# Kernel optimization log

Hardware: AMD Instinct MI355X
Metric: run time of the kernel (lower is better)

## Reference

```python
import jax, jax.numpy as jnp
import numpy as np

# Production-scale perfect decision-tree ensemble (Hummingbird perf_tree_trav layout)
B, F, T, D, C = 16384, 256, 512, 7, 4  # batch, features, trees, internal levels below root, classes


def setup_inputs() -> dict:
    key = jax.random.key(0)
    k = jax.random.split(key, 6)
    total = T * (2 ** (D + 1) - 2)  # concatenated per-level node/bias tables, level l has T*2^l entries
    return {
        "x": jax.random.normal(k[0], (B, F), dtype=jnp.float32),
        "root_nodes": jax.random.randint(k[1], (T,), 0, F, dtype=jnp.int32),
        "root_biases": jax.random.normal(k[2], (T,), dtype=jnp.float32),
        "tree_indices": jnp.arange(T, dtype=jnp.int32) * 2,
        "nodes_flat": jax.random.randint(k[3], (total,), 0, F, dtype=jnp.int32),
        "biases_flat": jax.random.normal(k[4], (total,), dtype=jnp.float32),
        "leaf_nodes": jax.random.normal(k[5], (T * 2 ** (D + 1), C), dtype=jnp.float32),
    }


def reference(x, root_nodes, root_biases, tree_indices, nodes_flat, biases_flat, leaf_nodes):
    # Root level: compare each tree's root feature against its bias. decision_cond = less (lt).
    # tree_indices = t*2 offsets indices into the flat level-1 table of size 2T;
    # the offset doubles along with the level size via `2*idx + cond`.
    idx = (x[:, root_nodes] < root_biases).astype(jnp.int32) + tree_indices  # [B, T]
    off = 0
    for l in range(1, D + 1):  # static loop over tree depth
        size = T << l
        lvl_nodes = nodes_flat[off:off + size]
        lvl_biases = biases_flat[off:off + size]
        feat_idx = lvl_nodes[idx]                          # [B, T] feature ids for current nodes
        feats = jnp.take_along_axis(x, feat_idx, axis=1)   # [B, T] per-sample feature gather
        idx = 2 * idx + (feats < lvl_biases[idx]).astype(jnp.int32)
        off += size
    leaves = leaf_nodes[idx]                               # [B, T, C]
    return leaves.sum(axis=1)                              # [B, C]
```

## Files before the change

kernel.cpp:

```cpp
#include <hip/hip_runtime.h>

#define BB 16384
#define FF 256
#define TT 512
#define DD 7

#define XS 257

constexpr int S_   = 32;
constexpr int NT_  = 512;
constexpr int NTG  = NT_ / S_;
constexpr int TPT  = TT / NTG;
constexpr int NP   = 8;
constexpr int NJ   = TPT / NP;
constexpr int NPACK = TT * ((1 << (DD + 1)) - 2);

__global__ void pack_nodes_kernel(const int* __restrict__ nf,
                                  const float* __restrict__ bf,
                                  int2* __restrict__ tp, int n) {
    int i = blockIdx.x * 256 + threadIdx.x;
    if (i < n) tp[i] = make_int2(nf[i], __float_as_int(bf[i]));
}

template<bool PACKED>
__global__ __launch_bounds__(NT_, 4)
void tree_traverse_kernel(const float* __restrict__ x,
                          const int*   __restrict__ root_nodes,
                          const float* __restrict__ root_biases,
                          const int*   __restrict__ nodes_flat,
                          const float* __restrict__ biases_flat,
                          const float* __restrict__ leaf_nodes,
                          const int2*  __restrict__ tp,
                          float*       __restrict__ out)
{
    __shared__ float x_s[S_ * XS];

    const int tid = threadIdx.x;
    const int s   = tid & (S_ - 1);
    const int tg  = tid / S_;
    const int s0  = blockIdx.x * S_;

    {
        const float4* xg = (const float4*)(x + (size_t)s0 * FF);
        const int r = tid >> 4;
        const int v = tid & 15;
        #pragma unroll
        for (int c = 0; c < 4; ++c) {
            const float4 q = xg[r * (FF / 4) + v + 16 * c];
            const int base = r * XS + (v + 16 * c) * 4;
            x_s[base + 0] = q.x; x_s[base + 1] = q.y;
            x_s[base + 2] = q.z; x_s[base + 3] = q.w;
        }
    }
    __syncthreads();

    const int xb = s * XS;
    const float4* leaf4 = (const float4*)leaf_nodes;
    float a0 = 0.f, a1 = 0.f, a2 = 0.f, a3 = 0.f;

    #pragma unroll 1
    for (int j = 0; j < NJ; ++j) {
        const int tbase = tg * TPT + j * NP;

        int p[NP];
        #pragma unroll
        for (int k = 0; k < NP; ++k) {
            const int t  = tbase + k;
            const int rn = root_nodes[t];
            const float rb = root_biases[t];
            p[k] = (x_s[xb + rn] < rb) ? 1 : 0;
        }

        #pragma unroll
        for (int l = 1; l <= DD; ++l) {
            const int lbase = TT * ((1 << l) - 2);
            #pragma unroll
            for (int k = 0; k < NP; ++k) {
                const int t = tbase + k;
                const int e = lbase + (t << l) + p[k];
                int   fi; float bi;
                if (PACKED) {
                    const int2 nb = tp[e];
                    fi = nb.x; bi = __int_as_float(nb.y);
                } else {
                    fi = nodes_flat[e]; bi = biases_flat[e];
                }
                const float ft = x_s[xb + fi];
                p[k] = 2 * p[k] + ((ft < bi) ? 1 : 0);
            }
        }

        #pragma unroll
        for (int k = 0; k < NP; ++k) {
            const int t = tbase + k;
            const float4 lf = leaf4[(t << (DD + 1)) + p[k]];
            a0 += lf.x; a1 += lf.y; a2 += lf.z; a3 += lf.w;
        }
    }

    __syncthreads();
    float* red = x_s;
    red[tid * 4 + 0] = a0; red[tid * 4 + 1] = a1;
    red[tid * 4 + 2] = a2; red[tid * 4 + 3] = a3;
    __syncthreads();
    if (tid < S_) {
        float o0 = 0.f, o1 = 0.f, o2 = 0.f, o3 = 0.f;
        #pragma unroll
        for (int g = 0; g < NTG; ++g) {
            const int jj = (g * S_ + tid) * 4;
            o0 += red[jj + 0]; o1 += red[jj + 1];
            o2 += red[jj + 2]; o3 += red[jj + 3];
        }
        ((float4*)out)[s0 + tid] = make_float4(o0, o1, o2, o3);
    }
}

extern "C" void kernel_launch(void* const* d_in, const int* in_sizes, int n_in,
                              void* d_out, int out_size, void* d_ws, size_t ws_size,
                              hipStream_t stream) {
    const float* x           = (const float*)d_in[0];
    const int*   root_nodes  = (const int*)  d_in[1];
    const float* root_biases = (const float*)d_in[2];
    const int*   nodes_flat  = (const int*)  d_in[4];
    const float* biases_flat = (const float*)d_in[5];
    const float* leaf_nodes  = (const float*)d_in[6];
    float*       out         = (float*)d_out;

    const bool packed = ws_size >= (size_t)NPACK * sizeof(int2);
    int2* tp = (int2*)d_ws;

    if (packed) {
        pack_nodes_kernel<<<(NPACK + 255) / 256, 256, 0, stream>>>(
            nodes_flat, biases_flat, tp, NPACK);
        tree_traverse_kernel<true><<<BB / S_, NT_, 0, stream>>>(
            x, root_nodes, root_biases, nodes_flat, biases_flat, leaf_nodes, tp, out);
    } else {
        tree_traverse_kernel<false><<<BB / S_, NT_, 0, stream>>>(
            x, root_nodes, root_biases, nodes_flat, biases_flat, leaf_nodes, tp, out);
    }
}
```

Baseline: 117.6 us.

## Split trees across two grid halves with atomic output reduction, drop node packing

Splits the tree ensemble into two halves along a second grid dimension, so each block traverses 256 trees for its 32 samples. Partial sums are combined with atomicAdd into an output that is zeroed by a memset first. The separate pack kernel that interleaved node ids and biases is removed in favour of two separate loads, and launch bounds are raised to 8 blocks per CU. This doubles the number of blocks, which helps occupancy and load balance, but loads the x tile into shared memory twice and adds atomics plus a memset.

```diff
diff --git a/kernel.cpp b/kernel.cpp
--- a/kernel.cpp
+++ b/kernel.cpp
@@ -10,27 +10,18 @@
 constexpr int S_   = 32;
 constexpr int NT_  = 512;
 constexpr int NTG  = NT_ / S_;
-constexpr int TPT  = TT / NTG;
+constexpr int HT   = TT / 2;
+constexpr int TPT  = HT / NTG;
 constexpr int NP   = 8;
 constexpr int NJ   = TPT / NP;
-constexpr int NPACK = TT * ((1 << (DD + 1)) - 2);
 
-__global__ void pack_nodes_kernel(const int* __restrict__ nf,
-                                  const float* __restrict__ bf,
-                                  int2* __restrict__ tp, int n) {
-    int i = blockIdx.x * 256 + threadIdx.x;
-    if (i < n) tp[i] = make_int2(nf[i], __float_as_int(bf[i]));
-}
-
-template<bool PACKED>
-__global__ __launch_bounds__(NT_, 4)
+__global__ __launch_bounds__(NT_, 8)
 void tree_traverse_kernel(const float* __restrict__ x,
                           const int*   __restrict__ root_nodes,
                           const float* __restrict__ root_biases,
                           const int*   __restrict__ nodes_flat,
                           const float* __restrict__ biases_flat,
                           const float* __restrict__ leaf_nodes,
-                          const int2*  __restrict__ tp,
                           float*       __restrict__ out)
 {
     __shared__ float x_s[S_ * XS];
@@ -39,6 +30,7 @@
     const int s   = tid & (S_ - 1);
     const int tg  = tid / S_;
     const int s0  = blockIdx.x * S_;
+    const int h0  = blockIdx.y * HT;
 
     {
         const float4* xg = (const float4*)(x + (size_t)s0 * FF);
@@ -60,7 +52,7 @@
 
     #pragma unroll 1
     for (int j = 0; j < NJ; ++j) {
-        const int tbase = tg * TPT + j * NP;
+        const int tbase = h0 + tg * TPT + j * NP;
 
         int p[NP];
         #pragma unroll
@@ -78,13 +70,8 @@
             for (int k = 0; k < NP; ++k) {
                 const int t = tbase + k;
                 const int e = lbase + (t << l) + p[k];
-                int   fi; float bi;
-                if (PACKED) {
-                    const int2 nb = tp[e];
-                    fi = nb.x; bi = __int_as_float(nb.y);
-                } else {
-                    fi = nodes_flat[e]; bi = biases_flat[e];
-                }
+                const int   fi = nodes_flat[e];
+                const float bi = biases_flat[e];
                 const float ft = x_s[xb + fi];
                 p[k] = 2 * p[k] + ((ft < bi) ? 1 : 0);
             }
@@ -103,15 +90,14 @@
     red[tid * 4 + 0] = a0; red[tid * 4 + 1] = a1;
     red[tid * 4 + 2] = a2; red[tid * 4 + 3] = a3;
     __syncthreads();
-    if (tid < S_) {
-        float o0 = 0.f, o1 = 0.f, o2 = 0.f, o3 = 0.f;
+    if (tid < S_ * 4) {
+        const int smp = tid >> 2;
+        const int c   = tid & 3;
+        float o = 0.f;
         #pragma unroll
-        for (int g = 0; g < NTG; ++g) {
-            const int jj = (g * S_ + tid) * 4;
-            o0 += red[jj + 0]; o1 += red[jj + 1];
-            o2 += red[jj + 2]; o3 += red[jj + 3];
-        }
-        ((float4*)out)[s0 + tid] = make_float4(o0, o1, o2, o3);
+        for (int g = 0; g < NTG; ++g)
+            o += red[((g << 5) + smp) * 4 + c];
+        atomicAdd(out + (size_t)(s0 + smp) * 4 + c, o);
     }
 }
 
@@ -126,16 +112,9 @@
     const float* leaf_nodes  = (const float*)d_in[6];
     float*       out         = (float*)d_out;
 
-    const bool packed = ws_size >= (size_t)NPACK * sizeof(int2);
-    int2* tp = (int2*)d_ws;
+    (void)hipMemsetAsync(d_out, 0, (size_t)out_size * sizeof(float), stream);
 
-    if (packed) {
-        pack_nodes_kernel<<<(NPACK + 255) / 256, 256, 0, stream>>>(
-            nodes_flat, biases_flat, tp, NPACK);
-        tree_traverse_kernel<true><<<BB / S_, NT_, 0, stream>>>(
-            x, root_nodes, root_biases, nodes_flat, biases_flat, leaf_nodes, tp, out);
-    } else {
-        tree_traverse_kernel<false><<<BB / S_, NT_, 0, stream>>>(
-            x, root_nodes, root_biases, nodes_flat, biases_flat, leaf_nodes, tp, out);
-    }
+    dim3 grid(BB / S_, 2);
+    tree_traverse_kernel<<<grid, NT_, 0, stream>>>(
+        x, root_nodes, root_biases, nodes_flat, biases_flat, leaf_nodes, out);
 }
```

Measured after the change: 134.9 us. +14.7%, slower.

## Use 64-sample blocks with XOR-swizzled LDS rows and packed root nodes

Applied to the files above, without the earlier changes.

Doubles samples per block to 64 with 1024 threads, so each 64-lane wavefront works on the same tree and its node-table loads hit a small, shared region. The padded LDS layout is replaced by an XOR swizzle on unpadded 256-float rows, sized through dynamic shared memory. Root feature/bias pairs are added to the packed int2 table so they come from one load. The final reduction is vectorized. The cost is a 64 KB LDS footprint and 1024-thread blocks under the existing launch-bounds occupancy hint, which may limit resident blocks or squeeze registers.

```diff
diff --git a/kernel.cpp b/kernel.cpp
--- a/kernel.cpp
+++ b/kernel.cpp
@@ -5,21 +5,26 @@
 #define TT 512
 #define DD 7
 
-#define XS 257
-
-constexpr int S_   = 32;
-constexpr int NT_  = 512;
+constexpr int S_   = 64;
+constexpr int NT_  = 1024;
 constexpr int NTG  = NT_ / S_;
 constexpr int TPT  = TT / NTG;
 constexpr int NP   = 8;
 constexpr int NJ   = TPT / NP;
 constexpr int NPACK = TT * ((1 << (DD + 1)) - 2);
+constexpr int NPALL = NPACK + TT;
 
 __global__ void pack_nodes_kernel(const int* __restrict__ nf,
                                   const float* __restrict__ bf,
-                                  int2* __restrict__ tp, int n) {
+                                  const int* __restrict__ rn,
+                                  const float* __restrict__ rb,
+                                  int2* __restrict__ tp) {
     int i = blockIdx.x * 256 + threadIdx.x;
-    if (i < n) tp[i] = make_int2(nf[i], __float_as_int(bf[i]));
+    if (i < NPACK) tp[i] = make_int2(nf[i], __float_as_int(bf[i]));
+    else if (i < NPALL) {
+        int t = i - NPACK;
+        tp[i] = make_int2(rn[t], __float_as_int(rb[t]));
+    }
 }
 
 template<bool PACKED>
@@ -33,28 +38,33 @@
                           const int2*  __restrict__ tp,
                           float*       __restrict__ out)
 {
-    __shared__ float x_s[S_ * XS];
+    extern __shared__ float x_s[];
 
     const int tid = threadIdx.x;
     const int s   = tid & (S_ - 1);
-    const int tg  = tid / S_;
+    const int tg  = tid >> 6;
     const int s0  = blockIdx.x * S_;
 
     {
         const float4* xg = (const float4*)(x + (size_t)s0 * FF);
-        const int r = tid >> 4;
-        const int v = tid & 15;
+        const int r  = tid >> 4;
+        const int v  = tid & 15;
+        const int rz = r & 31;
+        float* row = x_s + (r << 8);
         #pragma unroll
         for (int c = 0; c < 4; ++c) {
             const float4 q = xg[r * (FF / 4) + v + 16 * c];
-            const int base = r * XS + (v + 16 * c) * 4;
-            x_s[base + 0] = q.x; x_s[base + 1] = q.y;
-            x_s[base + 2] = q.z; x_s[base + 3] = q.w;
+            const int f0 = (v + 16 * c) * 4;
+            row[(f0 + 0) ^ rz] = q.x;
+            row[(f0 + 1) ^ rz] = q.y;
+            row[(f0 + 2) ^ rz] = q.z;
+            row[(f0 + 3) ^ rz] = q.w;
         }
     }
     __syncthreads();
 
-    const int xb = s * XS;
+    const int   xb = s << 8;
+    const int   sz = s & 31;
     const float4* leaf4 = (const float4*)leaf_nodes;
     float a0 = 0.f, a1 = 0.f, a2 = 0.f, a3 = 0.f;
 
@@ -65,10 +75,15 @@
         int p[NP];
         #pragma unroll
         for (int k = 0; k < NP; ++k) {
-            const int t  = tbase + k;
-            const int rn = root_nodes[t];
-            const float rb = root_biases[t];
-            p[k] = (x_s[xb + rn] < rb) ? 1 : 0;
+            const int t = tbase + k;
+            int rn; float rbv;
+            if (PACKED) {
+                const int2 nb = tp[NPACK + t];
+                rn = nb.x; rbv = __int_as_float(nb.y);
+            } else {
+                rn = root_nodes[t]; rbv = root_biases[t];
+            }
+            p[k] = (x_s[xb | (rn ^ sz)] < rbv) ? 1 : 0;
         }
 
         #pragma unroll
@@ -78,14 +93,14 @@
             for (int k = 0; k < NP; ++k) {
                 const int t = tbase + k;
                 const int e = lbase + (t << l) + p[k];
-                int   fi; float bi;
+                int fi; float bi;
                 if (PACKED) {
                     const int2 nb = tp[e];
                     fi = nb.x; bi = __int_as_float(nb.y);
                 } else {
                     fi = nodes_flat[e]; bi = biases_flat[e];
                 }
-                const float ft = x_s[xb + fi];
+                const float ft = x_s[xb | (fi ^ sz)];
                 p[k] = 2 * p[k] + ((ft < bi) ? 1 : 0);
             }
         }
@@ -99,19 +114,14 @@
     }
 
     __syncthreads();
-    float* red = x_s;
-    red[tid * 4 + 0] = a0; red[tid * 4 + 1] = a1;
-    red[tid * 4 + 2] = a2; red[tid * 4 + 3] = a3;
+    ((float4*)x_s)[tid] = make_float4(a0, a1, a2, a3);
     __syncthreads();
-    if (tid < S_) {
-        float o0 = 0.f, o1 = 0.f, o2 = 0.f, o3 = 0.f;
+    if (tid < S_ * 4) {
+        float o = 0.f;
         #pragma unroll
-        for (int g = 0; g < NTG; ++g) {
-            const int jj = (g * S_ + tid) * 4;
-            o0 += red[jj + 0]; o1 += red[jj + 1];
-            o2 += red[jj + 2]; o3 += red[jj + 3];
-        }
-        ((float4*)out)[s0 + tid] = make_float4(o0, o1, o2, o3);
+        for (int g = 0; g < NTG; ++g)
+            o += x_s[(g << 8) + tid];
+        out[(size_t)s0 * 4 + tid] = o;
     }
 }
 
@@ -126,16 +136,17 @@
     const float* leaf_nodes  = (const float*)d_in[6];
     float*       out         = (float*)d_out;
 
-    const bool packed = ws_size >= (size_t)NPACK * sizeof(int2);
+    constexpr size_t LDS_BYTES = (size_t)S_ * FF * sizeof(float);
+    const bool packed = ws_size >= (size_t)NPALL * sizeof(int2);
     int2* tp = (int2*)d_ws;
 
     if (packed) {
-        pack_nodes_kernel<<<(NPACK + 255) / 256, 256, 0, stream>>>(
-            nodes_flat, biases_flat, tp, NPACK);
-        tree_traverse_kernel<true><<<BB / S_, NT_, 0, stream>>>(
+        pack_nodes_kernel<<<(NPALL + 255) / 256, 256, 0, stream>>>(
+            nodes_flat, biases_flat, root_nodes, root_biases, tp);
+        tree_traverse_kernel<true><<<BB / S_, NT_, LDS_BYTES, stream>>>(
             x, root_nodes, root_biases, nodes_flat, biases_flat, leaf_nodes, tp, out);
     } else {
-        tree_traverse_kernel<false><<<BB / S_, NT_, 0, stream>>>(
+        tree_traverse_kernel<false><<<BB / S_, NT_, LDS_BYTES, stream>>>(
             x, root_nodes, root_biases, nodes_flat, biases_flat, leaf_nodes, tp, out);
     }
 }
```

Result: no change. 115.4 us (-1.9%).
